# Kernel tuning notes

Hardware: AMD Instinct MI355X
Metric: run time of the kernel (lower is better)

The kernel has to match this reference:

```python
import jax, jax.numpy as jnp
import numpy as np
from jax import lax

EPS = 1e-06
QP_ITERS = 500  # unrolled mirror-descent iterations for the simplex QP


def mlp_embed(x, W1, b1, W2, b2):
    # embedding_net: 2-layer MLP, [B, N, in_dim] -> [B, N, embed_dim]
    h = jax.nn.relu(jnp.einsum('bni,ih->bnh', x, W1) + b1)
    return jnp.einsum('bnh,hd->bnd', h, W2) + b2


def batch_svdd(emb, eps):
    # emb: [B, S, D].  SVDD dual QP per task:
    #   min_a  a^T K a - diag(K)^T a   s.t.  a >= 0, sum(a) = 1
    # (Q = 2K, p = -diag(K), G = -I, h = 0, A = 1^T, b = 1 in the torch QPFunction call)
    B, S, D = emb.shape
    K = jnp.einsum('bsd,btd->bst', emb, emb) + eps * jnp.eye(S, dtype=emb.dtype)
    kdiag = jnp.diagonal(K, axis1=-2, axis2=-1)  # [B, S]
    # Solve on the simplex with exponentiated-gradient (mirror descent with KL),
    # which converges to the unique QP optimum (K is PD after the eps jitter).
    # Per-task step size from the Gershgorin bound: eta <= 1 / (2 * ||K||_inf).
    eta = 1.0 / (2.0 * jnp.max(jnp.sum(jnp.abs(K), axis=-1), axis=-1, keepdims=True))  # [B,1]
    a0 = jnp.full((B, S), 1.0 / S, dtype=emb.dtype)

    def step(a, _):
        g = 2.0 * jnp.einsum('bst,bt->bs', K, a) - kdiag  # grad of a^T K a - kdiag^T a
        a = jax.nn.softmax(jnp.log(a + 1e-30) - eta * g, axis=-1)
        return a, None

    alphas, _ = lax.scan(step, a0, None, length=QP_ITERS)
    centers = jnp.einsum('bs,bsd->bd', alphas, emb)  # sum(alphas * inputs, dim=1)
    return centers


def setup_inputs() -> dict:
    key = jax.random.key(0)
    ks = jax.random.split(key, 4)
    tasks, shot, n_query, in_dim, hid, emb = 256, 32, 64, 1024, 2048, 512
    support_inputs = jax.random.normal(ks[0], (tasks, shot, in_dim), jnp.float32)
    query_inputs = jax.random.normal(ks[1], (tasks, n_query, in_dim), jnp.float32)
    W1 = jax.random.normal(ks[2], (in_dim, hid), jnp.float32) / np.sqrt(in_dim)
    b1 = jnp.zeros((hid,), jnp.float32)
    W2 = jax.random.normal(ks[3], (hid, emb), jnp.float32) / np.sqrt(hid)
    b2 = jnp.zeros((emb,), jnp.float32)
    return {'support_inputs': support_inputs, 'query_inputs': query_inputs,
            'W1': W1, 'b1': b1, 'W2': W2, 'b2': b2}


def reference(support_inputs, query_inputs, W1, b1, W2, b2):
    support_emb = mlp_embed(support_inputs, W1, b1, W2, b2)  # [B, S, D]
    centers = batch_svdd(support_emb, EPS)                   # [B, D]
    query_emb = mlp_embed(query_inputs, W1, b1, W2, b2)      # [B, Q, D]
    logits = -jnp.sum((centers[:, None, :] - query_emb) ** 2, axis=-1)  # [B, Q]
    return logits
```

## Files before the change

### kernel.cpp

```cpp
#include <hip/hip_runtime.h>
#include <hip/hip_bf16.h>

typedef __attribute__((ext_vector_type(8))) short bf16x8;
typedef __attribute__((ext_vector_type(4))) float f32x4;
typedef __attribute__((ext_vector_type(4))) unsigned short us4;

__device__ __forceinline__ unsigned short bf16_rne(float f) {
  unsigned u = __float_as_uint(f);
  unsigned r = u + 0x7fffu + ((u >> 16) & 1u);
  return (unsigned short)(r >> 16);
}

__device__ __forceinline__ void gload16(const void* g, void* l) {
  typedef const __attribute__((address_space(1))) unsigned int* gas;
  typedef __attribute__((address_space(3))) unsigned int* las;
  __builtin_amdgcn_global_load_lds((gas)g, (las)l, 16, 0, 0);
}

__device__ __forceinline__ float lane_f(float v, int l) {
  return __int_as_float(__builtin_amdgcn_readlane(__float_as_int(v), l));
}

template <int CTRL>
__device__ __forceinline__ float dpp_add(float x) {
  return x + __int_as_float(__builtin_amdgcn_update_dpp(0, __float_as_int(x), CTRL, 0xf, 0xf, true));
}

#define BAR() asm volatile("s_barrier" ::: "memory")
#define VMCNT0() asm volatile("s_waitcnt vmcnt(0)" ::: "memory")
#define LGKM4() asm volatile("s_waitcnt lgkmcnt(4)" ::: "memory")
#define LGKM0() asm volatile("s_waitcnt lgkmcnt(0)" ::: "memory")
#define SB() __builtin_amdgcn_sched_barrier(0)

__global__ __launch_bounds__(256) void castx(const float* __restrict__ sup,
                                             const float* __restrict__ qry,
                                             unsigned short* __restrict__ X) {
  const int stride = gridDim.x * blockDim.x;
  for (int i = blockIdx.x * blockDim.x + threadIdx.x; i < 6291456; i += stride) {
    float4 v = (i < 2097152) ? ((const float4*)sup)[i] : ((const float4*)qry)[i - 2097152];
    us4 o = { bf16_rne(v.x), bf16_rne(v.y), bf16_rne(v.z), bf16_rne(v.w) };
    *(us4*)(X + (size_t)i * 4) = o;
  }
}

__global__ __launch_bounds__(256) void transcast(const float* __restrict__ src,
                                                 unsigned short* __restrict__ dst,
                                                 int R, int C) {
  __shared__ float t[32][33];
  const int tx = threadIdx.x & 31, ty = threadIdx.x >> 5;
  const int c0 = blockIdx.x * 32, r0 = blockIdx.y * 32;
#pragma unroll
  for (int j = 0; j < 4; j++)
    t[ty + j * 8][tx] = src[(size_t)(r0 + ty + j * 8) * C + c0 + tx];
  __syncthreads();
#pragma unroll
  for (int j = 0; j < 4; j++)
    dst[(size_t)(c0 + ty + j * 8) * R + r0 + tx] = bf16_rne(t[tx][ty + j * 8]);
}

#define MFMA_Q(AO, BO, MOFF, NOFF)                                                  \
  __builtin_amdgcn_s_setprio(1);                                                    \
  _Pragma("unroll") for (int i_ = 0; i_ < 4; ++i_)                                  \
  _Pragma("unroll") for (int j_ = 0; j_ < 2; ++j_)                                  \
  _Pragma("unroll") for (int ks_ = 0; ks_ < 2; ++ks_)                               \
    acc[(MOFF) + i_][(NOFF) + j_] = __builtin_amdgcn_mfma_f32_16x16x32_bf16(        \
        AO[i_][ks_], BO[j_][ks_], acc[(MOFF) + i_][(NOFF) + j_], 0, 0, 0);          \
  __builtin_amdgcn_s_setprio(0);

#define RDA(KS, ACH, MH, I) \
  (*(const bf16x8*)(lsc + ((ACH) * 32768 + (MH) * 8192 + (I) * 2048) + ((KS) ? vA_1 : vA_0)))
#define RDB(KS, BCH, JI) \
  (*(const bf16x8*)(lsc + ((BCH) * 32768 + (JI) * 2048) + ((KS) ? vB_1 : vB_0)))

#define STG(GLP, CHOFF, HALF)                                                     \
  gload16((GLP) + (size_t)((HALF) * 128) * ld,                                    \
          (char*)ls + ((CHOFF) + (HALF) * 16384) + wid * 1024);                   \
  gload16((GLP) + (size_t)((HALF) * 128 + 64) * ld,                               \
          (char*)ls + ((CHOFF) + (HALF) * 16384 + 8192) + wid * 1024);

#define TILE(ACH, BCH, ASO, BSO, T)                                               \
  {                                                                               \
    VMCNT0();                                                                     \
    BAR();                                                                        \
    _Pragma("unroll") for (int i = 0; i < 4; ++i) {                               \
      afr[i][0] = RDA(0, ACH, 0, i); afr[i][1] = RDA(1, ACH, 0, i);               \
    }                                                                             \
    _Pragma("unroll") for (int j = 0; j < 2; ++j) {                               \
      bfr0[j][0] = RDB(0, BCH, j); bfr0[j][1] = RDB(1, BCH, j);                   \
    }                                                                             \
    _Pragma("unroll") for (int j = 0; j < 2; ++j) {                               \
      bfr1[j][0] = RDB(0, BCH, 2 + j); bfr1[j][1] = RDB(1, BCH, 2 + j);           \
    }                                                                             \
    const char* Ap_ = AgL + (size_t)(T) * 128;                                    \
    const char* Bp_ = BgL + (size_t)(T) * 128;                                    \
    STG(Ap_, ASO, 0); STG(Ap_, ASO, 1);                                           \
    STG(Bp_, BSO, 0); STG(Bp_, BSO, 1);                                           \
    LGKM4(); SB();                                                                \
    MFMA_Q(afr, bfr0, 0, 0);                                                      \
    LGKM0(); SB();                                                                \
    MFMA_Q(afr, bfr1, 0, 2);                                                      \
    _Pragma("unroll") for (int i = 0; i < 4; ++i) {                               \
      afr[i][0] = RDA(0, ACH, 1, i); afr[i][1] = RDA(1, ACH, 1, i);               \
    }                                                                             \
    LGKM0(); SB();                                                                \
    MFMA_Q(afr, bfr1, 4, 2);                                                      \
    MFMA_Q(afr, bfr0, 4, 0);                                                      \
  }

template <int ACT, int OUTBF>
__global__ __launch_bounds__(512) void gemm256(const unsigned short* __restrict__ A,
                                               const unsigned short* __restrict__ BT,
                                               const float* __restrict__ bias,
                                               void* __restrict__ Cout,
                                               int M, int N, int K) {
  __shared__ __attribute__((aligned(16))) short ls[4][16384];
  const int tid = threadIdx.x, lane = tid & 63, wid = tid >> 6;
  const int wm = wid >> 2, wn = wid & 3;
  const int l15 = lane & 15, lg = lane >> 4;

  int lin = blockIdx.y * gridDim.x + blockIdx.x;
  int nwg = gridDim.x * gridDim.y;
  int swz = (lin & 7) * (nwg >> 3) + (lin >> 3);
  int bx = swz % gridDim.x, by = swz / gridDim.x;
  const int m0 = by * 256, n0 = bx * 256;

  const size_t ld = (size_t)K * 2;
  const char* Ag = (const char*)A + (size_t)m0 * ld;
  const char* Bg = (const char*)BT + (size_t)n0 * ld;
  const int NT = K >> 6;
  const char* lsc = (const char*)ls;

  const int swz4 = (l15 & 7) << 4;
  const int bk0 = (l15 * 128 + lg * 16) ^ swz4;
  const int bk1 = (l15 * 128 + 64 + lg * 16) ^ swz4;
  const int vA_0 = bk0 + wm * 16384, vA_1 = bk1 + wm * 16384;
  const int vB_0 = bk0 + wn * 8192 + 65536, vB_1 = bk1 + wn * 8192 + 65536;

  const int srow = wid * 8 + (lane >> 3);
  const int kperm = ((lane & 7) ^ (lane >> 3)) << 4;
  const char* AgL = Ag + (size_t)srow * ld + kperm;
  const char* BgL = Bg + (size_t)srow * ld + kperm;

  f32x4 acc[8][4] = {};
  bf16x8 afr[4][2], bfr0[2][2], bfr1[2][2];

  STG(AgL, 0, 0); STG(AgL, 0, 1);
  STG(BgL, 65536, 0); STG(BgL, 65536, 1);

  for (int u = 0; u < NT; u += 2) {
    int t1 = u + 1;
    int t2 = u + 2; if (t2 >= NT) t2 = 0;
    TILE(0, 0, 32768, 98304, t1);
    TILE(1, 1, 0, 65536, t2);
  }

  float bv[4];
#pragma unroll
  for (int nf = 0; nf < 4; ++nf) bv[nf] = bias[n0 + wn * 64 + nf * 16 + l15];
#pragma unroll
  for (int mf = 0; mf < 8; ++mf) {
    int rbase = m0 + wm * 128 + mf * 16 + lg * 4;
#pragma unroll
    for (int nf = 0; nf < 4; ++nf) {
      int col = n0 + wn * 64 + nf * 16 + l15;
#pragma unroll
      for (int j = 0; j < 4; ++j) {
        float v = acc[mf][nf][j] + bv[nf];
        if (ACT) v = v > 0.f ? v : 0.f;
        size_t idx = (size_t)(rbase + j) * N + col;
        if (OUTBF) ((unsigned short*)Cout)[idx] = bf16_rne(v);
        else       ((float*)Cout)[idx] = v;
      }
    }
  }
}

#define MFMA_T(AO, BO, MOFF, NOFF)                                                  \
  __builtin_amdgcn_s_setprio(1);                                                    \
  _Pragma("unroll") for (int i_ = 0; i_ < 3; ++i_)                                  \
  _Pragma("unroll") for (int j_ = 0; j_ < 2; ++j_)                                  \
  _Pragma("unroll") for (int ks_ = 0; ks_ < 2; ++ks_)                               \
    acc[(MOFF) + i_][(NOFF) + j_] = __builtin_amdgcn_mfma_f32_16x16x32_bf16(        \
        AO[i_][ks_], BO[j_][ks_], acc[(MOFF) + i_][(NOFF) + j_], 0, 0, 0);          \
  __builtin_amdgcn_s_setprio(0);

#define RA2(KS, ACH, MH, I) \
  (*(const bf16x8*)(lsc + ((ACH) * 24576 + (MH) * 6144 + (I) * 2048) + ((KS) ? vA_1 : vA_0)))
#define RB2(KS, BCH, JI) \
  (*(const bf16x8*)(lsc + ((BCH) * 32768 + (JI) * 2048) + ((KS) ? vB_1 : vB_0)))

#define STGA2(CHOFF, T)                                                           \
  {                                                                               \
    const char* p_ = AgL + (size_t)(T) * 128;                                     \
    gload16(p_,               (char*)ls + (CHOFF) + wid * 3072);                  \
    gload16(p_ + 8 * ld,      (char*)ls + (CHOFF) + wid * 3072 + 1024);           \
    gload16(p_ + 16 * ld,     (char*)ls + (CHOFF) + wid * 3072 + 2048);           \
  }
#define STGB2(CHOFF, T)                                                           \
  {                                                                               \
    const char* p_ = BgL + (size_t)(T) * 128;                                     \
    gload16(p_,               (char*)ls + (CHOFF) + wid * 4096);                  \
    gload16(p_ + 8 * ld,      (char*)ls + (CHOFF) + wid * 4096 + 1024);           \
    gload16(p_ + 16 * ld,     (char*)ls + (CHOFF) + wid * 4096 + 2048);           \
    gload16(p_ + 24 * ld,     (char*)ls + (CHOFF) + wid * 4096 + 3072);           \
  }

#define TILE2(ACH, BCH, ASO, BSO, T)                                              \
  {                                                                               \
    VMCNT0();                                                                     \
    BAR();                                                                        \
    _Pragma("unroll") for (int i = 0; i < 3; ++i) {                               \
      afl[i][0] = RA2(0, ACH, 0, i); afl[i][1] = RA2(1, ACH, 0, i);               \
    }                                                                             \
    _Pragma("unroll") for (int j = 0; j < 2; ++j) {                               \
      bfr0[j][0] = RB2(0, BCH, j); bfr0[j][1] = RB2(1, BCH, j);                   \
    }                                                                             \
    _Pragma("unroll") for (int j = 0; j < 2; ++j) {                               \
      bfr1[j][0] = RB2(0, BCH, 2 + j); bfr1[j][1] = RB2(1, BCH, 2 + j);           \
    }                                                                             \
    STGA2(ASO, T); STGB2(BSO, T);                                                 \
    LGKM4(); SB();                                                                \
    MFMA_T(afl, bfr0, 0, 0);                                                      \
    LGKM0(); SB();                                                                \
    MFMA_T(afl, bfr1, 0, 2);                                                      \
    _Pragma("unroll") for (int i = 0; i < 3; ++i) {                               \
      afl[i][0] = RA2(0, ACH, 1, i); afl[i][1] = RA2(1, ACH, 1, i);               \
    }                                                                             \
    LGKM0(); SB();                                                                \
    MFMA_T(afl, bfr1, 3, 2);                                                      \
    MFMA_T(afl, bfr0, 3, 0);                                                      \
  }

__global__ __launch_bounds__(512) void gemm192(const unsigned short* __restrict__ A,
                                               const unsigned short* __restrict__ BT,
                                               const float* __restrict__ bias,
                                               float* __restrict__ Cout) {
  __shared__ __attribute__((aligned(16))) short ls[57344];
  const int tid = threadIdx.x, lane = tid & 63, wid = tid >> 6;
  const int wm = wid >> 2, wn = wid & 3;
  const int l15 = lane & 15, lg = lane >> 4;

  int lin = blockIdx.y * gridDim.x + blockIdx.x;
  int nwg = gridDim.x * gridDim.y;
  int swz = (lin & 7) * (nwg >> 3) + (lin >> 3);
  int bx = swz % gridDim.x, by = swz / gridDim.x;
  const int m0 = by * 192, n0 = bx * 256;

  constexpr int K = 2048;
  const size_t ld = (size_t)K * 2;
  const char* Ag = (const char*)A + (size_t)m0 * ld;
  const char* Bg = (const char*)BT + (size_t)n0 * ld;
  constexpr int NT = K >> 6;
  const char* lsc = (const char*)ls;

  const int swz4 = (l15 & 7) << 4;
  const int bk0 = (l15 * 128 + lg * 16) ^ swz4;
  const int bk1 = (l15 * 128 + 64 + lg * 16) ^ swz4;
  const int vA_0 = bk0 + wm * 12288, vA_1 = bk1 + wm * 12288;
  const int vB_0 = bk0 + wn * 8192 + 49152, vB_1 = bk1 + wn * 8192 + 49152;

  const int kperm = ((lane & 7) ^ (lane >> 3)) << 4;
  const char* AgL = Ag + (size_t)(wid * 24 + (lane >> 3)) * ld + kperm;
  const char* BgL = Bg + (size_t)(wid * 32 + (lane >> 3)) * ld + kperm;

  f32x4 acc[6][4] = {};
  bf16x8 afl[3][2], bfr0[2][2], bfr1[2][2];

  STGA2(0, 0);
  STGB2(49152, 0);

  for (int u = 0; u < NT; u += 2) {
    int t1 = u + 1;
    int t2 = u + 2; if (t2 >= NT) t2 = 0;
    TILE2(0, 0, 24576, 81920, t1);
    TILE2(1, 1, 0, 49152, t2);
  }

  float bv[4];
#pragma unroll
  for (int nf = 0; nf < 4; ++nf) bv[nf] = bias[n0 + wn * 64 + nf * 16 + l15];
#pragma unroll
  for (int mf = 0; mf < 6; ++mf) {
    int rbase = m0 + wm * 96 + mf * 16 + lg * 4;
#pragma unroll
    for (int nf = 0; nf < 4; ++nf) {
      int col = n0 + wn * 64 + nf * 16 + l15;
#pragma unroll
      for (int j = 0; j < 4; ++j)
        Cout[(size_t)(rbase + j) * 512 + col] = acc[mf][nf][j] + bv[nf];
    }
  }
}

__global__ __launch_bounds__(256) void makeK(const float* __restrict__ E,
                                             float* __restrict__ Km,
                                             float* __restrict__ eta2v) {
  __shared__ float es[32][512];
  const int b = blockIdx.x, tid = threadIdx.x;
  const float4* Eb = (const float4*)(E + (size_t)b * 32 * 512);
  float4* es4 = (float4*)&es[0][0];
  for (int i = tid; i < 32 * 128; i += 256) es4[i] = Eb[i];
  __syncthreads();

  const int s = tid >> 3, tq = tid & 7;
  const float4* rs4 = (const float4*)&es[s][0];
  const float4* rt0 = (const float4*)&es[tq * 4 + 0][0];
  const float4* rt1 = (const float4*)&es[tq * 4 + 1][0];
  const float4* rt2 = (const float4*)&es[tq * 4 + 2][0];
  const float4* rt3 = (const float4*)&es[tq * 4 + 3][0];
  float4 a0 = {0, 0, 0, 0}, a1 = {0, 0, 0, 0}, a2 = {0, 0, 0, 0}, a3 = {0, 0, 0, 0};
  for (int dd = 0; dd < 128; ++dd) {
    float4 av = rs4[dd];
    float4 b0 = rt0[dd], b1 = rt1[dd], b2 = rt2[dd], b3 = rt3[dd];
    a0.x = fmaf(av.x, b0.x, a0.x); a0.y = fmaf(av.y, b0.y, a0.y);
    a0.z = fmaf(av.z, b0.z, a0.z); a0.w = fmaf(av.w, b0.w, a0.w);
    a1.x = fmaf(av.x, b1.x, a1.x); a1.y = fmaf(av.y, b1.y, a1.y);
    a1.z = fmaf(av.z, b1.z, a1.z); a1.w = fmaf(av.w, b1.w, a1.w);
    a2.x = fmaf(av.x, b2.x, a2.x); a2.y = fmaf(av.y, b2.y, a2.y);
    a2.z = fmaf(av.z, b2.z, a2.z); a2.w = fmaf(av.w, b2.w, a2.w);
    a3.x = fmaf(av.x, b3.x, a3.x); a3.y = fmaf(av.y, b3.y, a3.y);
    a3.z = fmaf(av.z, b3.z, a3.z); a3.w = fmaf(av.w, b3.w, a3.w);
  }
  float kv[4] = { (a0.x + a0.y) + (a0.z + a0.w), (a1.x + a1.y) + (a1.z + a1.w),
                  (a2.x + a2.y) + (a2.z + a2.w), (a3.x + a3.y) + (a3.z + a3.w) };
  float p = 0.f;
#pragma unroll
  for (int j = 0; j < 4; j++) {
    if (s == tq * 4 + j) kv[j] += 1e-6f;
    p += fabsf(kv[j]);
    Km[(size_t)b * 1024 + s * 32 + tq * 4 + j] = kv[j];
  }
  p += __shfl_xor(p, 1); p += __shfl_xor(p, 2); p += __shfl_xor(p, 4);
  __syncthreads();
  float* rs = &es[0][0];
  if (tq == 0) rs[s] = p;
  __syncthreads();
  if (tid < 32) {
    float m = rs[tid];
    m = fmaxf(m, __shfl_xor(m, 1));
    m = fmaxf(m, __shfl_xor(m, 2));
    m = fmaxf(m, __shfl_xor(m, 4));
    m = fmaxf(m, __shfl_xor(m, 8));
    m = fmaxf(m, __shfl_xor(m, 16));
    if (tid == 0) eta2v[b] = 1.4426950408889634f / (2.0f * m);
  }
}

__global__ __launch_bounds__(256) void qp_kernel(const float* __restrict__ Km,
                                                 const float* __restrict__ eta2v,
                                                 float* __restrict__ alp) {
  const int lane = threadIdx.x & 63, wid = threadIdx.x >> 6;
  const int b = blockIdx.x * 4 + wid;
  const int s = lane & 31;
  const float* Kb = Km + (size_t)b * 1024;
  float kr[32];
#pragma unroll
  for (int i = 0; i < 8; i++) {
    float4 v = ((const float4*)(Kb + s * 32))[i];
    kr[i * 4 + 0] = v.x; kr[i * 4 + 1] = v.y; kr[i * 4 + 2] = v.z; kr[i * 4 + 3] = v.w;
  }
  const float kd = Kb[s * 33];
  const float eta2 = eta2v[b];
  const float c2p = fmaf(eta2, kd, 1.0f);
  const float m4n = -4.0f * eta2;
  float w = 0.03125f;
  for (int it = 0; it < 500; ++it) {
    float c0 = 0.f, c1 = 0.f, c2 = 0.f, c3 = 0.f, c4 = 0.f, c5 = 0.f, c6 = 0.f, c7 = 0.f;
#pragma unroll
    for (int t = 0; t < 4; ++t) {
      c0 = fmaf(kr[t],      lane_f(w, t),      c0);
      c1 = fmaf(kr[4 + t],  lane_f(w, 4 + t),  c1);
      c2 = fmaf(kr[8 + t],  lane_f(w, 8 + t),  c2);
      c3 = fmaf(kr[12 + t], lane_f(w, 12 + t), c3);
      c4 = fmaf(kr[16 + t], lane_f(w, 16 + t), c4);
      c5 = fmaf(kr[20 + t], lane_f(w, 20 + t), c5);
      c6 = fmaf(kr[24 + t], lane_f(w, 24 + t), c6);
      c7 = fmaf(kr[28 + t], lane_f(w, 28 + t), c7);
    }
    float tK = (((c0 + c1) + (c2 + c3)) + ((c4 + c5) + (c6 + c7)));
    float r = w;
    r = dpp_add<0x128>(r);
    r = dpp_add<0x124>(r);
    r = dpp_add<0x122>(r);
    r = dpp_add<0x121>(r);
    r = dpp_add<0x142>(r);
    r = dpp_add<0x143>(r);
    float R2 = __builtin_amdgcn_rcpf(lane_f(r, 63));
    float z = fmaf(m4n * R2, tK, c2p);
    w = (w * R2) * __builtin_amdgcn_exp2f(z);
  }
  float r = w;
  r = dpp_add<0x128>(r);
  r = dpp_add<0x124>(r);
  r = dpp_add<0x122>(r);
  r = dpp_add<0x121>(r);
  r = dpp_add<0x142>(r);
  r = dpp_add<0x143>(r);
  float R2 = __builtin_amdgcn_rcpf(lane_f(r, 63));
  if (lane < 32) alp[(size_t)b * 32 + s] = 2.0f * w * R2;
}

__global__ __launch_bounds__(128) void centers_k(const float* __restrict__ alp,
                                                 const float* __restrict__ E,
                                                 float* __restrict__ ctr) {
  const int b = blockIdx.x, t = threadIdx.x;
  __shared__ float av[32];
  if (t < 32) av[t] = alp[(size_t)b * 32 + t];
  __syncthreads();
  const float4* Eb = (const float4*)(E + (size_t)b * 32 * 512);
  float4 c = {0, 0, 0, 0};
#pragma unroll 8
  for (int sIdx = 0; sIdx < 32; sIdx++) {
    float a = av[sIdx];
    float4 v = Eb[sIdx * 128 + t];
    c.x = fmaf(a, v.x, c.x); c.y = fmaf(a, v.y, c.y);
    c.z = fmaf(a, v.z, c.z); c.w = fmaf(a, v.w, c.w);
  }
  ((float4*)ctr)[b * 128 + t] = c;
}

__global__ __launch_bounds__(256) void logits_k(const float* __restrict__ ctr,
                                                const float* __restrict__ E,
                                                float* __restrict__ out) {
  const int b = blockIdx.x, lane = threadIdx.x & 63, w = threadIdx.x >> 6;
  const float4* C4 = (const float4*)(ctr + (size_t)b * 512);
  const float4 cA = C4[lane * 2], cB = C4[lane * 2 + 1];
  const float4* Q4 = (const float4*)(E + (size_t)(8192 + b * 64) * 512);
  for (int q = w; q < 64; q += 4) {
    float4 e0 = Q4[(size_t)q * 128 + lane * 2];
    float4 e1 = Q4[(size_t)q * 128 + lane * 2 + 1];
    float d, ss = 0.f;
    d = cA.x - e0.x; ss = fmaf(d, d, ss);
    d = cA.y - e0.y; ss = fmaf(d, d, ss);
    d = cA.z - e0.z; ss = fmaf(d, d, ss);
    d = cA.w - e0.w; ss = fmaf(d, d, ss);
    d = cB.x - e1.x; ss = fmaf(d, d, ss);
    d = cB.y - e1.y; ss = fmaf(d, d, ss);
    d = cB.z - e1.z; ss = fmaf(d, d, ss);
    d = cB.w - e1.w; ss = fmaf(d, d, ss);
    ss += __shfl_xor(ss, 1);  ss += __shfl_xor(ss, 2);  ss += __shfl_xor(ss, 4);
    ss += __shfl_xor(ss, 8);  ss += __shfl_xor(ss, 16); ss += __shfl_xor(ss, 32);
    if (lane == 0) out[b * 64 + q] = -ss;
  }
}

extern "C" void kernel_launch(void* const* d_in, const int* in_sizes, int n_in,
                              void* d_out, int out_size, void* d_ws, size_t ws_size,
                              hipStream_t stream) {
  const float* sup = (const float*)d_in[0];
  const float* qry = (const float*)d_in[1];
  const float* W1  = (const float*)d_in[2];
  const float* b1  = (const float*)d_in[3];
  const float* W2  = (const float*)d_in[4];
  const float* b2  = (const float*)d_in[5];
  float* out = (float*)d_out;

  char* ws = (char*)d_ws;
  unsigned short* H   = (unsigned short*)(ws);
  unsigned short* Xbf = (unsigned short*)(ws + 100663296);
  float* E    = (float*)(ws + 100663296);
  unsigned short* W1T = (unsigned short*)(ws + 150994944);
  unsigned short* W2T = (unsigned short*)(ws + 155189248);
  float* Km   = (float*)(ws + 157286400);
  float* eta2 = (float*)(ws + 158334976);
  float* alp  = (float*)(ws + 158336000);
  float* ctr  = (float*)(ws + 158368768);

  castx<<<dim3(2048), dim3(256), 0, stream>>>(sup, qry, Xbf);
  transcast<<<dim3(64, 32), dim3(256), 0, stream>>>(W1, W1T, 1024, 2048);
  transcast<<<dim3(16, 64), dim3(256), 0, stream>>>(W2, W2T, 2048, 512);
  gemm256<1, 1><<<dim3(8, 96), dim3(512), 0, stream>>>(Xbf, W1T, b1, (void*)H, 24576, 2048, 1024);
  gemm192<<<dim3(2, 128), dim3(512), 0, stream>>>(H, W2T, b2, E);
  makeK<<<dim3(256), dim3(256), 0, stream>>>(E, Km, eta2);
  qp_kernel<<<dim3(64), dim3(256), 0, stream>>>(Km, eta2, alp);
  centers_k<<<dim3(256), dim3(128), 0, stream>>>(alp, E, ctr);
  logits_k<<<dim3(256), dim3(256), 0, stream>>>(ctr, E, out);
}
```

Measured before the change: 298.6 us.

## Fuse fp32-to-bf16 input cast into first GEMM's A-tile load path

Removes the separate castx kernel and has the first GEMM load fp32 support/query rows directly into registers, convert them to bf16, and write them into LDS. This drops one full pass that wrote and re-read a bf16 copy of the inputs through global memory. In exchange, the A operand now moves through registers instead of direct global-to-LDS loads, which doubles the A bytes read per tile (fp32). The conversion and LDS write happen after the MFMAs, behind a full vmcnt wait, so memory latency may be exposed and register pressure is higher.

```diff
diff --git a/kernel.cpp b/kernel.cpp
--- a/kernel.cpp
+++ b/kernel.cpp
@@ -3,7 +3,9 @@
 
 typedef __attribute__((ext_vector_type(8))) short bf16x8;
 typedef __attribute__((ext_vector_type(4))) float f32x4;
+typedef __attribute__((ext_vector_type(4))) float f4v;
 typedef __attribute__((ext_vector_type(4))) unsigned short us4;
+typedef __attribute__((ext_vector_type(8))) unsigned short us8;
 
 __device__ __forceinline__ unsigned short bf16_rne(float f) {
   unsigned u = __float_as_uint(f);
@@ -31,17 +33,6 @@
 #define LGKM4() asm volatile("s_waitcnt lgkmcnt(4)" ::: "memory")
 #define LGKM0() asm volatile("s_waitcnt lgkmcnt(0)" ::: "memory")
 #define SB() __builtin_amdgcn_sched_barrier(0)
-
-__global__ __launch_bounds__(256) void castx(const float* __restrict__ sup,
-                                             const float* __restrict__ qry,
-                                             unsigned short* __restrict__ X) {
-  const int stride = gridDim.x * blockDim.x;
-  for (int i = blockIdx.x * blockDim.x + threadIdx.x; i < 6291456; i += stride) {
-    float4 v = (i < 2097152) ? ((const float4*)sup)[i] : ((const float4*)qry)[i - 2097152];
-    us4 o = { bf16_rne(v.x), bf16_rne(v.y), bf16_rne(v.z), bf16_rne(v.w) };
-    *(us4*)(X + (size_t)i * 4) = o;
-  }
-}
 
 __global__ __launch_bounds__(256) void transcast(const float* __restrict__ src,
                                                  unsigned short* __restrict__ dst,
@@ -72,15 +63,40 @@
 #define RDB(KS, BCH, JI) \
   (*(const bf16x8*)(lsc + ((BCH) * 32768 + (JI) * 2048) + ((KS) ? vB_1 : vB_0)))
 
-#define STG(GLP, CHOFF, HALF)                                                     \
-  gload16((GLP) + (size_t)((HALF) * 128) * ld,                                    \
-          (char*)ls + ((CHOFF) + (HALF) * 16384) + wid * 1024);                   \
-  gload16((GLP) + (size_t)((HALF) * 128 + 64) * ld,                               \
-          (char*)ls + ((CHOFF) + (HALF) * 16384 + 8192) + wid * 1024);
-
-#define TILE(ACH, BCH, ASO, BSO, T)                                               \
-  {                                                                               \
-    VMCNT0();                                                                     \
+#define STGB(CHOFF, T)                                                            \
+  {                                                                               \
+    const char* Bp_ = BgL + (size_t)(T) * 128;                                    \
+    gload16(Bp_,                (char*)ls + (CHOFF) + wid * 1024);                \
+    gload16(Bp_ + 64 * ld,      (char*)ls + (CHOFF) + 8192 + wid * 1024);         \
+    gload16(Bp_ + 128 * ld,     (char*)ls + (CHOFF) + 16384 + wid * 1024);        \
+    gload16(Bp_ + 192 * ld,     (char*)ls + (CHOFF) + 24576 + wid * 1024);        \
+  }
+
+#define LOADA(T)                                                                  \
+  {                                                                               \
+    const char* p_ = AgF + (size_t)(T) * 256;                                     \
+    _Pragma("unroll") for (int r = 0; r < 4; ++r) {                               \
+      const char* q_ = p_ + (size_t)((r >> 1) * 128 + (r & 1) * 64) * 4096;       \
+      rg[2 * r]     = *(const f4v*)q_;                                            \
+      rg[2 * r + 1] = *(const f4v*)(q_ + 16);                                     \
+    }                                                                             \
+  }
+
+#define CVTWR(ASO)                                                                \
+  {                                                                               \
+    _Pragma("unroll") for (int r = 0; r < 4; ++r) {                               \
+      us8 v_;                                                                     \
+      _Pragma("unroll") for (int e = 0; e < 4; ++e) {                             \
+        v_[e]     = bf16_rne(rg[2 * r][e]);                                       \
+        v_[4 + e] = bf16_rne(rg[2 * r + 1][e]);                                   \
+      }                                                                           \
+      *(us8*)((char*)ls + (ASO) + (r >> 1) * 16384 + (r & 1) * 8192 +             \
+              wid * 1024 + lane * 16) = v_;                                       \
+    }                                                                             \
+  }
+
+#define TILE_F(ACH, BCH, ASO, BSO, T)                                             \
+  {                                                                               \
     BAR();                                                                        \
     _Pragma("unroll") for (int i = 0; i < 4; ++i) {                               \
       afr[i][0] = RDA(0, ACH, 0, i); afr[i][1] = RDA(1, ACH, 0, i);               \
@@ -91,10 +107,8 @@
     _Pragma("unroll") for (int j = 0; j < 2; ++j) {                               \
       bfr1[j][0] = RDB(0, BCH, 2 + j); bfr1[j][1] = RDB(1, BCH, 2 + j);           \
     }                                                                             \
-    const char* Ap_ = AgL + (size_t)(T) * 128;                                    \
-    const char* Bp_ = BgL + (size_t)(T) * 128;                                    \
-    STG(Ap_, ASO, 0); STG(Ap_, ASO, 1);                                           \
-    STG(Bp_, BSO, 0); STG(Bp_, BSO, 1);                                           \
+    STGB(BSO, T);                                                                 \
+    LOADA(T);                                                                     \
     LGKM4(); SB();                                                                \
     MFMA_Q(afr, bfr0, 0, 0);                                                      \
     LGKM0(); SB();                                                                \
@@ -105,14 +119,16 @@
     LGKM0(); SB();                                                                \
     MFMA_Q(afr, bfr1, 4, 2);                                                      \
     MFMA_Q(afr, bfr0, 4, 0);                                                      \
-  }
-
-template <int ACT, int OUTBF>
-__global__ __launch_bounds__(512) void gemm256(const unsigned short* __restrict__ A,
-                                               const unsigned short* __restrict__ BT,
-                                               const float* __restrict__ bias,
-                                               void* __restrict__ Cout,
-                                               int M, int N, int K) {
+    VMCNT0(); SB();                                                               \
+    CVTWR(ASO);                                                                   \
+    LGKM0();                                                                      \
+  }
+
+__global__ __launch_bounds__(512) void gemm1f(const float* __restrict__ sup,
+                                              const float* __restrict__ qry,
+                                              const unsigned short* __restrict__ W1T,
+                                              const float* __restrict__ bias,
+                                              unsigned short* __restrict__ H) {
   __shared__ __attribute__((aligned(16))) short ls[4][16384];
   const int tid = threadIdx.x, lane = tid & 63, wid = tid >> 6;
   const int wm = wid >> 2, wn = wid & 3;
@@ -124,10 +140,10 @@
   int bx = swz % gridDim.x, by = swz / gridDim.x;
   const int m0 = by * 256, n0 = bx * 256;
 
+  constexpr int K = 1024;
   const size_t ld = (size_t)K * 2;
-  const char* Ag = (const char*)A + (size_t)m0 * ld;
-  const char* Bg = (const char*)BT + (size_t)n0 * ld;
-  const int NT = K >> 6;
+  const char* Bg = (const char*)W1T + (size_t)n0 * ld;
+  constexpr int NT = K >> 6;
   const char* lsc = (const char*)ls;
 
   const int swz4 = (l15 & 7) << 4;
@@ -138,20 +154,27 @@
 
   const int srow = wid * 8 + (lane >> 3);
   const int kperm = ((lane & 7) ^ (lane >> 3)) << 4;
-  const char* AgL = Ag + (size_t)srow * ld + kperm;
   const char* BgL = Bg + (size_t)srow * ld + kperm;
+
+  const char* Asrc = (m0 < 8192) ? (const char*)sup + (size_t)m0 * 4096
+                                 : (const char*)qry + (size_t)(m0 - 8192) * 4096;
+  const char* AgF = Asrc + (size_t)srow * 4096 + (size_t)kperm * 2;
 
   f32x4 acc[8][4] = {};
   bf16x8 afr[4][2], bfr0[2][2], bfr1[2][2];
-
-  STG(AgL, 0, 0); STG(AgL, 0, 1);
-  STG(BgL, 65536, 0); STG(BgL, 65536, 1);
+  f4v rg[8];
+
+  STGB(65536, 0);
+  LOADA(0);
+  VMCNT0();
+  CVTWR(0);
+  LGKM0();
 
   for (int u = 0; u < NT; u += 2) {
     int t1 = u + 1;
     int t2 = u + 2; if (t2 >= NT) t2 = 0;
-    TILE(0, 0, 32768, 98304, t1);
-    TILE(1, 1, 0, 65536, t2);
+    TILE_F(0, 0, 32768, 98304, t1);
+    TILE_F(1, 1, 0, 65536, t2);
   }
 
   float bv[4];
@@ -166,10 +189,8 @@
 #pragma unroll
       for (int j = 0; j < 4; ++j) {
         float v = acc[mf][nf][j] + bv[nf];
-        if (ACT) v = v > 0.f ? v : 0.f;
-        size_t idx = (size_t)(rbase + j) * N + col;
-        if (OUTBF) ((unsigned short*)Cout)[idx] = bf16_rne(v);
-        else       ((float*)Cout)[idx] = v;
+        v = v > 0.f ? v : 0.f;
+        H[(size_t)(rbase + j) * 2048 + col] = bf16_rne(v);
       }
     }
   }
@@ -457,7 +478,6 @@
 
   char* ws = (char*)d_ws;
   unsigned short* H   = (unsigned short*)(ws);
-  unsigned short* Xbf = (unsigned short*)(ws + 100663296);
   float* E    = (float*)(ws + 100663296);
   unsigned short* W1T = (unsigned short*)(ws + 150994944);
   unsigned short* W2T = (unsigned short*)(ws + 155189248);
@@ -466,10 +486,9 @@
   float* alp  = (float*)(ws + 158336000);
   float* ctr  = (float*)(ws + 158368768);
 
-  castx<<<dim3(2048), dim3(256), 0, stream>>>(sup, qry, Xbf);
   transcast<<<dim3(64, 32), dim3(256), 0, stream>>>(W1, W1T, 1024, 2048);
   transcast<<<dim3(16, 64), dim3(256), 0, stream>>>(W2, W2T, 2048, 512);
-  gemm256<1, 1><<<dim3(8, 96), dim3(512), 0, stream>>>(Xbf, W1T, b1, (void*)H, 24576, 2048, 1024);
+  gemm1f<<<dim3(8, 96), dim3(512), 0, stream>>>(sup, qry, W1T, b1, H);
   gemm192<<<dim3(2, 128), dim3(512), 0, stream>>>(H, W2T, b2, E);
   makeK<<<dim3(256), dim3(256), 0, stream>>>(E, Km, eta2);
   qp_kernel<<<dim3(64), dim3(256), 0, stream>>>(Km, eta2, alp);
```

Result: no change. 302.1 us (+1.2%).

## Restructure first GEMM into eight-phase pipelined loop with finer-grained staging

Applied to the files above, without the earlier changes.

Replaces the templated two-stage gemm256 with a specialized gemm1_8p kernel for the first MLP layer. It splits each 64-wide K tile into quarter-phases that interleave LDS fragment reads, half-tile global-to-LDS loads and MFMA groups, using partial vmcnt/lgkmcnt waits instead of a full drain per tile. The B buffers are laid out so the next B tile can be prefetched while A is still in use. K and N are hardcoded, and the many extra barriers per phase add synchronization overhead.

```diff
diff --git a/kernel.cpp b/kernel.cpp
--- a/kernel.cpp
+++ b/kernel.cpp
@@ -28,6 +28,8 @@
 
 #define BAR() asm volatile("s_barrier" ::: "memory")
 #define VMCNT0() asm volatile("s_waitcnt vmcnt(0)" ::: "memory")
+#define VMCNT4() asm volatile("s_waitcnt vmcnt(4)" ::: "memory")
+#define LGKM8() asm volatile("s_waitcnt lgkmcnt(8)" ::: "memory")
 #define LGKM4() asm volatile("s_waitcnt lgkmcnt(4)" ::: "memory")
 #define LGKM0() asm volatile("s_waitcnt lgkmcnt(0)" ::: "memory")
 #define SB() __builtin_amdgcn_sched_barrier(0)
@@ -67,53 +69,27 @@
         AO[i_][ks_], BO[j_][ks_], acc[(MOFF) + i_][(NOFF) + j_], 0, 0, 0);          \
   __builtin_amdgcn_s_setprio(0);
 
-#define RDA(KS, ACH, MH, I) \
-  (*(const bf16x8*)(lsc + ((ACH) * 32768 + (MH) * 8192 + (I) * 2048) + ((KS) ? vA_1 : vA_0)))
-#define RDB(KS, BCH, JI) \
-  (*(const bf16x8*)(lsc + ((BCH) * 32768 + (JI) * 2048) + ((KS) ? vB_1 : vB_0)))
-
-#define STG(GLP, CHOFF, HALF)                                                     \
-  gload16((GLP) + (size_t)((HALF) * 128) * ld,                                    \
-          (char*)ls + ((CHOFF) + (HALF) * 16384) + wid * 1024);                   \
-  gload16((GLP) + (size_t)((HALF) * 128 + 64) * ld,                               \
-          (char*)ls + ((CHOFF) + (HALF) * 16384 + 8192) + wid * 1024);
-
-#define TILE(ACH, BCH, ASO, BSO, T)                                               \
-  {                                                                               \
-    VMCNT0();                                                                     \
-    BAR();                                                                        \
-    _Pragma("unroll") for (int i = 0; i < 4; ++i) {                               \
-      afr[i][0] = RDA(0, ACH, 0, i); afr[i][1] = RDA(1, ACH, 0, i);               \
-    }                                                                             \
-    _Pragma("unroll") for (int j = 0; j < 2; ++j) {                               \
-      bfr0[j][0] = RDB(0, BCH, j); bfr0[j][1] = RDB(1, BCH, j);                   \
-    }                                                                             \
-    _Pragma("unroll") for (int j = 0; j < 2; ++j) {                               \
-      bfr1[j][0] = RDB(0, BCH, 2 + j); bfr1[j][1] = RDB(1, BCH, 2 + j);           \
-    }                                                                             \
-    const char* Ap_ = AgL + (size_t)(T) * 128;                                    \
-    const char* Bp_ = BgL + (size_t)(T) * 128;                                    \
-    STG(Ap_, ASO, 0); STG(Ap_, ASO, 1);                                           \
-    STG(Bp_, BSO, 0); STG(Bp_, BSO, 1);                                           \
-    LGKM4(); SB();                                                                \
-    MFMA_Q(afr, bfr0, 0, 0);                                                      \
-    LGKM0(); SB();                                                                \
-    MFMA_Q(afr, bfr1, 0, 2);                                                      \
-    _Pragma("unroll") for (int i = 0; i < 4; ++i) {                               \
-      afr[i][0] = RDA(0, ACH, 1, i); afr[i][1] = RDA(1, ACH, 1, i);               \
-    }                                                                             \
-    LGKM0(); SB();                                                                \
-    MFMA_Q(afr, bfr1, 4, 2);                                                      \
-    MFMA_Q(afr, bfr0, 4, 0);                                                      \
-  }
-
-template <int ACT, int OUTBF>
-__global__ __launch_bounds__(512) void gemm256(const unsigned short* __restrict__ A,
-                                               const unsigned short* __restrict__ BT,
-                                               const float* __restrict__ bias,
-                                               void* __restrict__ Cout,
-                                               int M, int N, int K) {
-  __shared__ __attribute__((aligned(16))) short ls[4][16384];
+#define RD_A8(BUF, QM)                                                              \
+  _Pragma("unroll") for (int i = 0; i < 4; ++i) {                                   \
+    afr[i][0] = *(const bf16x8*)(lsc + (BUF) * 32768 + ((QM) * 4 + i) * 2048 + vA_0); \
+    afr[i][1] = *(const bf16x8*)(lsc + (BUF) * 32768 + ((QM) * 4 + i) * 2048 + vA_1); \
+  }
+#define RD_B4(BUF, QN, DST)                                                         \
+  _Pragma("unroll") for (int j = 0; j < 2; ++j) {                                   \
+    DST[j][0] = *(const bf16x8*)(lsc + (BUF) * 32768 + ((QN) * 2 + j) * 2048 + vB_0); \
+    DST[j][1] = *(const bf16x8*)(lsc + (BUF) * 32768 + ((QN) * 2 + j) * 2048 + vB_1); \
+  }
+#define STGH(CHOFF, GPTR, H, T)                                                     \
+  gload16((GPTR) + (size_t)((H) * 128) * ld + (size_t)(T) * 128,                    \
+          (char*)ls + (CHOFF) + wid * 1024);                                        \
+  gload16((GPTR) + (size_t)((H) * 128 + 64) * ld + (size_t)(T) * 128,               \
+          (char*)ls + (CHOFF) + 8192 + wid * 1024);
+
+__global__ __launch_bounds__(512) void gemm1_8p(const unsigned short* __restrict__ A,
+                                                const unsigned short* __restrict__ BT,
+                                                const float* __restrict__ bias,
+                                                unsigned short* __restrict__ H) {
+  __shared__ __attribute__((aligned(16))) short ls[65536];
   const int tid = threadIdx.x, lane = tid & 63, wid = tid >> 6;
   const int wm = wid >> 2, wn = wid & 3;
   const int l15 = lane & 15, lg = lane >> 4;
@@ -124,17 +100,18 @@
   int bx = swz % gridDim.x, by = swz / gridDim.x;
   const int m0 = by * 256, n0 = bx * 256;
 
+  constexpr int K = 1024;
   const size_t ld = (size_t)K * 2;
   const char* Ag = (const char*)A + (size_t)m0 * ld;
   const char* Bg = (const char*)BT + (size_t)n0 * ld;
-  const int NT = K >> 6;
   const char* lsc = (const char*)ls;
 
   const int swz4 = (l15 & 7) << 4;
   const int bk0 = (l15 * 128 + lg * 16) ^ swz4;
   const int bk1 = (l15 * 128 + 64 + lg * 16) ^ swz4;
   const int vA_0 = bk0 + wm * 16384, vA_1 = bk1 + wm * 16384;
-  const int vB_0 = bk0 + wn * 8192 + 65536, vB_1 = bk1 + wn * 8192 + 65536;
+  const int vB_0 = bk0 + (wn >> 1) * 16384 + (wn & 1) * 8192 + 65536;
+  const int vB_1 = bk1 + (wn >> 1) * 16384 + (wn & 1) * 8192 + 65536;
 
   const int srow = wid * 8 + (lane >> 3);
   const int kperm = ((lane & 7) ^ (lane >> 3)) << 4;
@@ -144,14 +121,58 @@
   f32x4 acc[8][4] = {};
   bf16x8 afr[4][2], bfr0[2][2], bfr1[2][2];
 
-  STG(AgL, 0, 0); STG(AgL, 0, 1);
-  STG(BgL, 65536, 0); STG(BgL, 65536, 1);
-
-  for (int u = 0; u < NT; u += 2) {
-    int t1 = u + 1;
-    int t2 = u + 2; if (t2 >= NT) t2 = 0;
-    TILE(0, 0, 32768, 98304, t1);
-    TILE(1, 1, 0, 65536, t2);
+  STGH(0, AgL, 0, 0);      STGH(16384, AgL, 1, 0);
+  STGH(65536, BgL, 0, 0);  STGH(81920, BgL, 1, 0);
+  STGH(98304, BgL, 0, 1);  STGH(114688, BgL, 1, 1);
+  VMCNT4();
+  BAR();
+
+  for (int it = 0; it < 8; ++it) {
+    const int t1 = 2 * it + 1;
+    int t2a = 2 * it + 2; if (t2a >= 16) t2a = 0;
+    int t2b = 2 * it + 3; if (t2b >= 16) t2b -= 16;
+    RD_A8(0, 0); RD_B4(0, 0, bfr0);
+    STGH(32768, AgL, 0, t1);
+    LGKM8();
+    BAR(); LGKM0(); SB();
+    MFMA_Q(afr, bfr0, 0, 0);
+    BAR();
+    RD_B4(0, 1, bfr1);
+    STGH(49152, AgL, 1, t1);
+    BAR(); LGKM0(); SB();
+    MFMA_Q(afr, bfr1, 0, 2);
+    BAR();
+    RD_A8(0, 1);
+    STGH(65536, BgL, 0, t2a);
+    BAR(); LGKM0(); SB();
+    MFMA_Q(afr, bfr1, 4, 2);
+    BAR();
+    STGH(81920, BgL, 1, t2a);
+    VMCNT4();
+    BAR(); SB();
+    MFMA_Q(afr, bfr0, 4, 0);
+    BAR();
+    RD_A8(1, 0); RD_B4(1, 0, bfr0);
+    STGH(0, AgL, 0, t2a);
+    LGKM8();
+    BAR(); LGKM0(); SB();
+    MFMA_Q(afr, bfr0, 0, 0);
+    BAR();
+    RD_B4(1, 1, bfr1);
+    STGH(16384, AgL, 1, t2a);
+    BAR(); LGKM0(); SB();
+    MFMA_Q(afr, bfr1, 0, 2);
+    BAR();
+    RD_A8(1, 1);
+    STGH(98304, BgL, 0, t2b);
+    BAR(); LGKM0(); SB();
+    MFMA_Q(afr, bfr1, 4, 2);
+    BAR();
+    STGH(114688, BgL, 1, t2b);
+    VMCNT4();
+    BAR(); SB();
+    MFMA_Q(afr, bfr0, 4, 0);
+    BAR();
   }
 
   float bv[4];
@@ -166,10 +187,8 @@
 #pragma unroll
       for (int j = 0; j < 4; ++j) {
         float v = acc[mf][nf][j] + bv[nf];
-        if (ACT) v = v > 0.f ? v : 0.f;
-        size_t idx = (size_t)(rbase + j) * N + col;
-        if (OUTBF) ((unsigned short*)Cout)[idx] = bf16_rne(v);
-        else       ((float*)Cout)[idx] = v;
+        v = v > 0.f ? v : 0.f;
+        H[(size_t)(rbase + j) * 2048 + col] = bf16_rne(v);
       }
     }
   }
@@ -469,7 +488,7 @@
   castx<<<dim3(2048), dim3(256), 0, stream>>>(sup, qry, Xbf);
   transcast<<<dim3(64, 32), dim3(256), 0, stream>>>(W1, W1T, 1024, 2048);
   transcast<<<dim3(16, 64), dim3(256), 0, stream>>>(W2, W2T, 2048, 512);
-  gemm256<1, 1><<<dim3(8, 96), dim3(512), 0, stream>>>(Xbf, W1T, b1, (void*)H, 24576, 2048, 1024);
+  gemm1_8p<<<dim3(8, 96), dim3(512), 0, stream>>>(Xbf, W1T, b1, H);
   gemm192<<<dim3(2, 128), dim3(512), 0, stream>>>(H, W2T, b2, E);
   makeK<<<dim3(256), dim3(256), 0, stream>>>(E, Km, eta2);
   qp_kernel<<<dim3(64), dim3(256), 0, stream>>>(Km, eta2, alp);
```

After: 301.9 us. About the same (+1.1%).

## Triple-buffer A tiles in gemm192 so loads stay in flight across barriers

Applied to the files above, without the earlier changes.

Restructures the gemm192 main loop from a double-buffered pair-unrolled pipeline to a rotating scheme: A uses three LDS buffers prefetched two tiles ahead, B uses two buffers one tile ahead. The wait before each barrier becomes vmcnt(3), so the newest A prefetch can stay outstanding while the current tile is computed, hiding more global latency. LDS grows to 136 KB, which limits occupancy to one 512-thread block per CU and relies on the larger LDS available on MI355X.

```diff
diff --git a/kernel.cpp b/kernel.cpp
--- a/kernel.cpp
+++ b/kernel.cpp
@@ -28,6 +28,7 @@
 
 #define BAR() asm volatile("s_barrier" ::: "memory")
 #define VMCNT0() asm volatile("s_waitcnt vmcnt(0)" ::: "memory")
+#define VMCNT3() asm volatile("s_waitcnt vmcnt(3)" ::: "memory")
 #define LGKM4() asm volatile("s_waitcnt lgkmcnt(4)" ::: "memory")
 #define LGKM0() asm volatile("s_waitcnt lgkmcnt(0)" ::: "memory")
 #define SB() __builtin_amdgcn_sched_barrier(0)
@@ -184,58 +185,32 @@
         AO[i_][ks_], BO[j_][ks_], acc[(MOFF) + i_][(NOFF) + j_], 0, 0, 0);          \
   __builtin_amdgcn_s_setprio(0);
 
-#define RA2(KS, ACH, MH, I) \
-  (*(const bf16x8*)(lsc + ((ACH) * 24576 + (MH) * 6144 + (I) * 2048) + ((KS) ? vA_1 : vA_0)))
-#define RB2(KS, BCH, JI) \
-  (*(const bf16x8*)(lsc + ((BCH) * 32768 + (JI) * 2048) + ((KS) ? vB_1 : vB_0)))
+#define RA2R(KS, MH, I) \
+  (*(const bf16x8*)(lsc + aR + (MH) * 6144 + (I) * 2048 + ((KS) ? vA_1 : vA_0)))
+#define RB2R(KS, JI) \
+  (*(const bf16x8*)(lsc + bR + (JI) * 2048 + ((KS) ? vB_1 : vB_0)))
 
 #define STGA2(CHOFF, T)                                                           \
   {                                                                               \
     const char* p_ = AgL + (size_t)(T) * 128;                                     \
-    gload16(p_,               (char*)ls + (CHOFF) + wid * 3072);                  \
-    gload16(p_ + 8 * ld,      (char*)ls + (CHOFF) + wid * 3072 + 1024);           \
-    gload16(p_ + 16 * ld,     (char*)ls + (CHOFF) + wid * 3072 + 2048);           \
+    gload16(p_,               lsw + (CHOFF) + wid * 3072);                        \
+    gload16(p_ + 8 * ld,      lsw + (CHOFF) + wid * 3072 + 1024);                 \
+    gload16(p_ + 16 * ld,     lsw + (CHOFF) + wid * 3072 + 2048);                 \
   }
 #define STGB2(CHOFF, T)                                                           \
   {                                                                               \
     const char* p_ = BgL + (size_t)(T) * 128;                                     \
-    gload16(p_,               (char*)ls + (CHOFF) + wid * 4096);                  \
-    gload16(p_ + 8 * ld,      (char*)ls + (CHOFF) + wid * 4096 + 1024);           \
-    gload16(p_ + 16 * ld,     (char*)ls + (CHOFF) + wid * 4096 + 2048);           \
-    gload16(p_ + 24 * ld,     (char*)ls + (CHOFF) + wid * 4096 + 3072);           \
-  }
-
-#define TILE2(ACH, BCH, ASO, BSO, T)                                              \
-  {                                                                               \
-    VMCNT0();                                                                     \
-    BAR();                                                                        \
-    _Pragma("unroll") for (int i = 0; i < 3; ++i) {                               \
-      afl[i][0] = RA2(0, ACH, 0, i); afl[i][1] = RA2(1, ACH, 0, i);               \
-    }                                                                             \
-    _Pragma("unroll") for (int j = 0; j < 2; ++j) {                               \
-      bfr0[j][0] = RB2(0, BCH, j); bfr0[j][1] = RB2(1, BCH, j);                   \
-    }                                                                             \
-    _Pragma("unroll") for (int j = 0; j < 2; ++j) {                               \
-      bfr1[j][0] = RB2(0, BCH, 2 + j); bfr1[j][1] = RB2(1, BCH, 2 + j);           \
-    }                                                                             \
-    STGA2(ASO, T); STGB2(BSO, T);                                                 \
-    LGKM4(); SB();                                                                \
-    MFMA_T(afl, bfr0, 0, 0);                                                      \
-    LGKM0(); SB();                                                                \
-    MFMA_T(afl, bfr1, 0, 2);                                                      \
-    _Pragma("unroll") for (int i = 0; i < 3; ++i) {                               \
-      afl[i][0] = RA2(0, ACH, 1, i); afl[i][1] = RA2(1, ACH, 1, i);               \
-    }                                                                             \
-    LGKM0(); SB();                                                                \
-    MFMA_T(afl, bfr1, 3, 2);                                                      \
-    MFMA_T(afl, bfr0, 3, 0);                                                      \
+    gload16(p_,               lsw + (CHOFF) + wid * 4096);                        \
+    gload16(p_ + 8 * ld,      lsw + (CHOFF) + wid * 4096 + 1024);                 \
+    gload16(p_ + 16 * ld,     lsw + (CHOFF) + wid * 4096 + 2048);                 \
+    gload16(p_ + 24 * ld,     lsw + (CHOFF) + wid * 4096 + 3072);                 \
   }
 
 __global__ __launch_bounds__(512) void gemm192(const unsigned short* __restrict__ A,
                                                const unsigned short* __restrict__ BT,
                                                const float* __restrict__ bias,
                                                float* __restrict__ Cout) {
-  __shared__ __attribute__((aligned(16))) short ls[57344];
+  __shared__ __attribute__((aligned(16))) char lsb[139264];
   const int tid = threadIdx.x, lane = tid & 63, wid = tid >> 6;
   const int wm = wid >> 2, wn = wid & 3;
   const int l15 = lane & 15, lg = lane >> 4;
@@ -251,13 +226,14 @@
   const char* Ag = (const char*)A + (size_t)m0 * ld;
   const char* Bg = (const char*)BT + (size_t)n0 * ld;
   constexpr int NT = K >> 6;
-  const char* lsc = (const char*)ls;
+  const char* lsc = (const char*)lsb;
+  char* lsw = (char*)lsb;
 
   const int swz4 = (l15 & 7) << 4;
   const int bk0 = (l15 * 128 + lg * 16) ^ swz4;
   const int bk1 = (l15 * 128 + 64 + lg * 16) ^ swz4;
   const int vA_0 = bk0 + wm * 12288, vA_1 = bk1 + wm * 12288;
-  const int vB_0 = bk0 + wn * 8192 + 49152, vB_1 = bk1 + wn * 8192 + 49152;
+  const int vB_0 = bk0 + wn * 8192, vB_1 = bk1 + wn * 8192;
 
   const int kperm = ((lane & 7) ^ (lane >> 3)) << 4;
   const char* AgL = Ag + (size_t)(wid * 24 + (lane >> 3)) * ld + kperm;
@@ -266,14 +242,45 @@
   f32x4 acc[6][4] = {};
   bf16x8 afl[3][2], bfr0[2][2], bfr1[2][2];
 
+  STGB2(73728, 0);
   STGA2(0, 0);
-  STGB2(49152, 0);
-
-  for (int u = 0; u < NT; u += 2) {
-    int t1 = u + 1;
-    int t2 = u + 2; if (t2 >= NT) t2 = 0;
-    TILE2(0, 0, 24576, 81920, t1);
-    TILE2(1, 1, 0, 49152, t2);
+  STGA2(24576, 1);
+
+  int aR = 0, aM = 24576, aS = 49152;
+  int bR = 73728, bS = 106496;
+
+  for (int u = 0; u < NT; ++u) {
+    VMCNT3();
+    BAR();
+#pragma unroll
+    for (int i = 0; i < 3; ++i) {
+      afl[i][0] = RA2R(0, 0, i); afl[i][1] = RA2R(1, 0, i);
+    }
+#pragma unroll
+    for (int j = 0; j < 2; ++j) {
+      bfr0[j][0] = RB2R(0, j); bfr0[j][1] = RB2R(1, j);
+    }
+#pragma unroll
+    for (int j = 0; j < 2; ++j) {
+      bfr1[j][0] = RB2R(0, 2 + j); bfr1[j][1] = RB2R(1, 2 + j);
+    }
+    int tb = u + 1; if (tb >= NT) tb = 0;
+    int ta = u + 2; if (ta >= NT) ta -= NT;
+    STGB2(bS, tb);
+    STGA2(aS, ta);
+    LGKM4(); SB();
+    MFMA_T(afl, bfr0, 0, 0);
+    LGKM0(); SB();
+    MFMA_T(afl, bfr1, 0, 2);
+#pragma unroll
+    for (int i = 0; i < 3; ++i) {
+      afl[i][0] = RA2R(0, 1, i); afl[i][1] = RA2R(1, 1, i);
+    }
+    LGKM0(); SB();
+    MFMA_T(afl, bfr1, 3, 2);
+    MFMA_T(afl, bfr0, 3, 0);
+    int t0 = aR; aR = aM; aM = aS; aS = t0;
+    int t1b = bR; bR = bS; bS = t1b;
   }
 
   float bv[4];
```

Result: no change. 301.5 us (+1.0%).
